# Performance work log

Hardware: AMD Instinct MI355X
Metric: run time of the kernel (lower is better)

Reference implementation:

```python
import jax, jax.numpy as jnp
import numpy as np

B, C, H, Wd = 16, 256, 64, 64
D_MODEL = 256


def setup_inputs() -> dict:
    key = jax.random.key(0)
    kx, kw = jax.random.split(key)
    x = jax.random.normal(kx, (B, C, H, Wd), dtype=jnp.float32)
    # 1x1 conv weight [out_c=1+2*d_model, in_c], scaled like kaiming-ish init
    W = jax.random.normal(kw, (1 + 2 * D_MODEL, C), dtype=jnp.float32) / np.sqrt(C)
    return {"x": x, "W": W}


def reference(x, W):
    b, c, h, w = x.shape
    d = (W.shape[0] - 1) // 2
    n = h * w
    xf = x.reshape(b, c, n)                      # [b, c, N]
    qkv = jnp.einsum('oc,bcn->bon', W, xf)       # 1x1 conv == channel GEMM
    q = qkv[:, :1]                               # [b, 1, N]
    k = qkv[:, 1:1 + d]                          # [b, d, N]
    v = qkv[:, 1 + d:]                           # [b, d, N]
    scores = jax.nn.softmax(q, axis=-1)          # softmax over tokens
    ctx = jnp.sum(k * scores, axis=-1, keepdims=True)  # [b, d, 1]
    out = jax.nn.relu(v) * ctx                   # gated ReLU(v)
    return out.reshape(b, d, h, w)
```

## Files before the change

### kernel.cpp

```cpp
#include <hip/hip_runtime.h>
#include <cstdint>
#include <cstddef>

#define NB 16
#define NC 256
#define NN 4096
#define ND 256

typedef unsigned short u16;
typedef unsigned int u32;

typedef __attribute__((ext_vector_type(8))) short short8;
typedef __attribute__((ext_vector_type(4))) float f32x4;

__device__ __forceinline__ u16 f2bf(float f) {
  union { float f; u32 u; } v; v.f = f;
  u32 r = v.u + 0x7FFFu + ((v.u >> 16) & 1u);
  return (u16)(r >> 16);
}

__global__ __launch_bounds__(256) void k_cast_transpose(const float* __restrict__ x,
                                                        u16* __restrict__ xbT) {
  __shared__ __align__(16) u16 tile[64 * 68];
  const int t = threadIdx.x;
  const int b = blockIdx.z, c0 = blockIdx.y * 64, n0 = blockIdx.x * 64;
  const float* xb = x + (size_t)(b * NC + c0) * NN + n0;
#pragma unroll
  for (int i = 0; i < 4; ++i) {
    int e = t + i * 256;
    int cl = e >> 4;
    int nl = (e & 15) * 4;
    float4 v = *(const float4*)(xb + (size_t)cl * NN + nl);
    tile[(nl + 0) * 68 + cl] = f2bf(v.x);
    tile[(nl + 1) * 68 + cl] = f2bf(v.y);
    tile[(nl + 2) * 68 + cl] = f2bf(v.z);
    tile[(nl + 3) * 68 + cl] = f2bf(v.w);
  }
  __syncthreads();
  u16* ob = xbT + (size_t)(b * NN + n0) * NC + c0;
#pragma unroll
  for (int i = 0; i < 4; ++i) {
    int e = t + i * 256;
    int nl = e >> 4;
    int cl = (e & 15) * 4;
    ushort4 pv = *(const ushort4*)&tile[nl * 68 + cl];
    *(ushort4*)(ob + (size_t)nl * NC + cl) = pv;
  }
}

__global__ __launch_bounds__(256) void k_q(const float* __restrict__ x,
                                           const float* __restrict__ W,
                                           float* __restrict__ q) {
  const int b = blockIdx.y;
  const int n = blockIdx.x * 256 + threadIdx.x;
  const float* xp = x + (size_t)b * NC * NN + n;
  float acc = 0.f;
#pragma unroll 16
  for (int c = 0; c < NC; ++c) acc += W[c] * xp[(size_t)c * NN];
  q[b * NN + n] = acc;
}

__global__ __launch_bounds__(256) void k_softmax(const float* __restrict__ q,
                                                 float* __restrict__ s) {
  __shared__ float red[256];
  const int b = blockIdx.x, t = threadIdx.x;
  const float* qb = q + b * NN;
  float v[16];
  float m = -3.4e38f;
#pragma unroll
  for (int i = 0; i < 16; ++i) { v[i] = qb[t + i * 256]; m = fmaxf(m, v[i]); }
  red[t] = m;
  __syncthreads();
  for (int off = 128; off > 0; off >>= 1) {
    if (t < off) red[t] = fmaxf(red[t], red[t + off]);
    __syncthreads();
  }
  const float M = red[0];
  __syncthreads();
  float sum = 0.f;
#pragma unroll
  for (int i = 0; i < 16; ++i) { v[i] = __expf(v[i] - M); sum += v[i]; }
  red[t] = sum;
  __syncthreads();
  for (int off = 128; off > 0; off >>= 1) {
    if (t < off) red[t] += red[t + off];
    __syncthreads();
  }
  const float inv = 1.f / red[0];
  float* sb = s + b * NN;
#pragma unroll
  for (int i = 0; i < 16; ++i) sb[t + i * 256] = v[i] * inv;
}

__global__ __launch_bounds__(256) void k_xs(const float* __restrict__ x,
                                            const float* __restrict__ s,
                                            float* __restrict__ xs) {
  __shared__ float red[256];
  const int c = blockIdx.x, b = blockIdx.y, t = threadIdx.x;
  const float* xp = x + (size_t)(b * NC + c) * NN;
  const float* sp = s + b * NN;
  float acc = 0.f;
#pragma unroll
  for (int i = 0; i < 16; ++i) { int n = t + i * 256; acc += xp[n] * sp[n]; }
  red[t] = acc;
  __syncthreads();
  for (int off = 128; off > 0; off >>= 1) {
    if (t < off) red[t] += red[t + off];
    __syncthreads();
  }
  if (t == 0) xs[b * NC + c] = red[0];
}

__global__ __launch_bounds__(256) void k_ctx(const float* __restrict__ W,
                                             const float* __restrict__ xs,
                                             float* __restrict__ ctx) {
  __shared__ float sx[NC];
  const int b = blockIdx.x, d = threadIdx.x;
  sx[d] = xs[b * NC + d];
  __syncthreads();
  const float* wk = W + (size_t)(1 + d) * NC;
  float acc = 0.f;
#pragma unroll 4
  for (int c = 0; c < NC; ++c) acc += wk[c] * sx[c];
  ctx[b * NC + d] = acc;
}

__global__ __launch_bounds__(256) void k_castwv(const float* __restrict__ W,
                                                u16* __restrict__ wvb) {
  const int i = (blockIdx.x * 256 + threadIdx.x) * 4;
  const float4 v = *(const float4*)(W + (size_t)(1 + ND) * NC + i);
  ushort4 o;
  o.x = f2bf(v.x); o.y = f2bf(v.y); o.z = f2bf(v.z); o.w = f2bf(v.w);
  *(ushort4*)(wvb + i) = o;
}

#define BM 128
#define BN 128
#define BK 32

__global__ __launch_bounds__(256) void k_gemm(const u16* __restrict__ xbT,
                                              const u16* __restrict__ wvb,
                                              const float* __restrict__ ctx,
                                              float* __restrict__ out) {
  __shared__ __align__(16) u16 As[BM * BK];
  __shared__ __align__(16) u16 Bs[BN * BK];
  const int t = threadIdx.x;
  const int b = blockIdx.z;
  const int d0 = blockIdx.y * BM;
  const int n0 = blockIdx.x * BN;
  const int lane = t & 63, w = t >> 6;
  const int wd = (w & 1) * 64, wn = (w >> 1) * 64;
  const int quad = lane >> 4, l15 = lane & 15;

  f32x4 acc[4][4];
#pragma unroll
  for (int mi = 0; mi < 4; ++mi)
#pragma unroll
    for (int ni = 0; ni < 4; ++ni)
      acc[mi][ni] = (f32x4){0.f, 0.f, 0.f, 0.f};

  const int row0 = t >> 2;
  const int qc8 = (t & 3) * 8;

  const u16* gA = wvb + (size_t)(d0 + row0) * NC + qc8;
  const u16* gB = xbT + (size_t)(b * NN + n0 + row0) * NC + qc8;
  u16* lA = &As[row0 * BK + qc8];
  u16* lB = &Bs[row0 * BK + qc8];

  for (int kk = 0; kk < NC; kk += BK) {
    __syncthreads();
#pragma unroll
    for (int i = 0; i < 2; ++i) {
      __builtin_amdgcn_global_load_lds(
          (const __attribute__((address_space(1))) u32*)(gA + kk + (size_t)(64 * i) * NC),
          (__attribute__((address_space(3))) u32*)(lA + 64 * i * BK), 16, 0, 0);
      __builtin_amdgcn_global_load_lds(
          (const __attribute__((address_space(1))) u32*)(gB + kk + (size_t)(64 * i) * NC),
          (__attribute__((address_space(3))) u32*)(lB + 64 * i * BK), 16, 0, 0);
    }
    __syncthreads();

    short8 af[4], bfr[4];
#pragma unroll
    for (int mi = 0; mi < 4; ++mi)
      af[mi] = *(const short8*)&As[(wd + mi * 16 + l15) * BK + quad * 8];
#pragma unroll
    for (int ni = 0; ni < 4; ++ni)
      bfr[ni] = *(const short8*)&Bs[(wn + ni * 16 + l15) * BK + quad * 8];
#pragma unroll
    for (int mi = 0; mi < 4; ++mi)
#pragma unroll
      for (int ni = 0; ni < 4; ++ni)
        acc[mi][ni] = __builtin_amdgcn_mfma_f32_16x16x32_bf16(af[mi], bfr[ni],
                                                              acc[mi][ni], 0, 0, 0);
  }

#pragma unroll
  for (int mi = 0; mi < 4; ++mi) {
#pragma unroll
    for (int r = 0; r < 4; ++r) {
      const int d = d0 + wd + mi * 16 + quad * 4 + r;
      const float cx = ctx[b * NC + d];
      float* op = out + (size_t)(b * NC + d) * NN + n0 + wn + l15;
#pragma unroll
      for (int ni = 0; ni < 4; ++ni) {
        float v = acc[mi][ni][r];
        op[ni * 16] = fmaxf(v, 0.f) * cx;
      }
    }
  }
}

extern "C" void kernel_launch(void* const* d_in, const int* in_sizes, int n_in,
                              void* d_out, int out_size, void* d_ws, size_t ws_size,
                              hipStream_t stream) {
  const float* x = (const float*)d_in[0];
  const float* W = (const float*)d_in[1];
  float* out = (float*)d_out;

  char* ws = (char*)d_ws;
  u16* xbT   = (u16*)ws;
  float* q   = (float*)(ws + 33554432);
  float* s   = (float*)(ws + 33554432 + 262144);
  float* xs  = (float*)(ws + 33554432 + 524288);
  float* ctx = (float*)(ws + 33554432 + 540672);
  u16* wvb   = (u16*)(ws + 33554432 + 557056);

  k_cast_transpose<<<dim3(64, 4, 16), 256, 0, stream>>>(x, xbT);
  k_q<<<dim3(16, 16), 256, 0, stream>>>(x, W, q);
  k_softmax<<<16, 256, 0, stream>>>(q, s);
  k_xs<<<dim3(256, 16), 256, 0, stream>>>(x, s, xs);
  k_ctx<<<16, 256, 0, stream>>>(W, xs, ctx);
  k_castwv<<<64, 256, 0, stream>>>(W, wvb);
  k_gemm<<<dim3(32, 2, 16), 256, 0, stream>>>(xbT, wvb, ctx, out);
}
```

Measured before the change: 175.7 us.

## Fuse q projection into cast-transpose, read bf16 xbT for xs, widen GEMM BK with swizzle

The q projection is computed inside the cast/transpose kernel from the already-loaded x tile and accumulated with atomics, so the separate pass over fp32 x is removed. The xs reduction now reads the half-size bf16 transposed copy instead of fp32 x and combines partial sums with atomics. The GEMM K-tile grows from 32 to 64 with an XOR-swizzled LDS layout, which halves the sync count and is meant to avoid bank conflicts. In exchange it adds a zeroing kernel and atomic accumulation, and xs now comes from bf16-rounded inputs, which loses some precision.

```diff
diff --git a/kernel.cpp b/kernel.cpp
--- a/kernel.cpp
+++ b/kernel.cpp
@@ -18,46 +18,58 @@
   u32 r = v.u + 0x7FFFu + ((v.u >> 16) & 1u);
   return (u16)(r >> 16);
 }
-
-__global__ __launch_bounds__(256) void k_cast_transpose(const float* __restrict__ x,
-                                                        u16* __restrict__ xbT) {
+__device__ __forceinline__ float bf2f(u16 h) {
+  union { u32 u; float f; } v; v.u = ((u32)h) << 16; return v.f;
+}
+
+__global__ __launch_bounds__(256) void k_zero(float* __restrict__ q,
+                                              float* __restrict__ xs) {
+  const int i = blockIdx.x * 256 + threadIdx.x;
+  if (i < NB * NN) q[i] = 0.f;
+  else xs[i - NB * NN] = 0.f;
+}
+
+__global__ __launch_bounds__(256) void k_cast_transpose_q(const float* __restrict__ x,
+                                                          const float* __restrict__ W,
+                                                          u16* __restrict__ xbT,
+                                                          float* __restrict__ q) {
   __shared__ __align__(16) u16 tile[64 * 68];
+  __shared__ float qred[16 * 64];
   const int t = threadIdx.x;
   const int b = blockIdx.z, c0 = blockIdx.y * 64, n0 = blockIdx.x * 64;
   const float* xb = x + (size_t)(b * NC + c0) * NN + n0;
+  const int nl = (t & 15) * 4;
+  float qacc[4] = {0.f, 0.f, 0.f, 0.f};
 #pragma unroll
   for (int i = 0; i < 4; ++i) {
-    int e = t + i * 256;
-    int cl = e >> 4;
-    int nl = (e & 15) * 4;
+    int cl = (t >> 4) + i * 16;
     float4 v = *(const float4*)(xb + (size_t)cl * NN + nl);
+    const float wq = W[c0 + cl];
+    qacc[0] += wq * v.x; qacc[1] += wq * v.y;
+    qacc[2] += wq * v.z; qacc[3] += wq * v.w;
     tile[(nl + 0) * 68 + cl] = f2bf(v.x);
     tile[(nl + 1) * 68 + cl] = f2bf(v.y);
     tile[(nl + 2) * 68 + cl] = f2bf(v.z);
     tile[(nl + 3) * 68 + cl] = f2bf(v.w);
   }
+#pragma unroll
+  for (int j = 0; j < 4; ++j) qred[(t >> 4) * 64 + nl + j] = qacc[j];
   __syncthreads();
   u16* ob = xbT + (size_t)(b * NN + n0) * NC + c0;
 #pragma unroll
   for (int i = 0; i < 4; ++i) {
     int e = t + i * 256;
-    int nl = e >> 4;
-    int cl = (e & 15) * 4;
-    ushort4 pv = *(const ushort4*)&tile[nl * 68 + cl];
-    *(ushort4*)(ob + (size_t)nl * NC + cl) = pv;
-  }
-}
-
-__global__ __launch_bounds__(256) void k_q(const float* __restrict__ x,
-                                           const float* __restrict__ W,
-                                           float* __restrict__ q) {
-  const int b = blockIdx.y;
-  const int n = blockIdx.x * 256 + threadIdx.x;
-  const float* xp = x + (size_t)b * NC * NN + n;
-  float acc = 0.f;
-#pragma unroll 16
-  for (int c = 0; c < NC; ++c) acc += W[c] * xp[(size_t)c * NN];
-  q[b * NN + n] = acc;
+    int rn = e >> 4;
+    int rc = (e & 15) * 4;
+    ushort4 pv = *(const ushort4*)&tile[rn * 68 + rc];
+    *(ushort4*)(ob + (size_t)rn * NC + rc) = pv;
+  }
+  if (t < 64) {
+    float s = 0.f;
+#pragma unroll
+    for (int k = 0; k < 16; ++k) s += qred[k * 64 + t];
+    atomicAdd(&q[b * NN + n0 + t], s);
+  }
 }
 
 __global__ __launch_bounds__(256) void k_softmax(const float* __restrict__ q,
@@ -92,23 +104,19 @@
   for (int i = 0; i < 16; ++i) sb[t + i * 256] = v[i] * inv;
 }
 
-__global__ __launch_bounds__(256) void k_xs(const float* __restrict__ x,
+__global__ __launch_bounds__(256) void k_xs(const u16* __restrict__ xbT,
                                             const float* __restrict__ s,
                                             float* __restrict__ xs) {
-  __shared__ float red[256];
-  const int c = blockIdx.x, b = blockIdx.y, t = threadIdx.x;
-  const float* xp = x + (size_t)(b * NC + c) * NN;
-  const float* sp = s + b * NN;
+  const int t = threadIdx.x;
+  const int b = blockIdx.y, n0 = blockIdx.x * 128;
+  const u16* xp = xbT + ((size_t)(b * NN + n0)) * NC + t;
+  const float* sp = s + b * NN + n0;
   float acc = 0.f;
-#pragma unroll
-  for (int i = 0; i < 16; ++i) { int n = t + i * 256; acc += xp[n] * sp[n]; }
-  red[t] = acc;
-  __syncthreads();
-  for (int off = 128; off > 0; off >>= 1) {
-    if (t < off) red[t] += red[t + off];
-    __syncthreads();
-  }
-  if (t == 0) xs[b * NC + c] = red[0];
+#pragma unroll 8
+  for (int j = 0; j < 128; ++j) {
+    acc += bf2f(xp[(size_t)j * NC]) * sp[j];
+  }
+  atomicAdd(&xs[b * NC + t], acc);
 }
 
 __global__ __launch_bounds__(256) void k_ctx(const float* __restrict__ W,
@@ -136,7 +144,7 @@
 
 #define BM 128
 #define BN 128
-#define BK 32
+#define BK 64
 
 __global__ __launch_bounds__(256) void k_gemm(const u16* __restrict__ xbT,
                                               const u16* __restrict__ wvb,
@@ -159,40 +167,45 @@
     for (int ni = 0; ni < 4; ++ni)
       acc[mi][ni] = (f32x4){0.f, 0.f, 0.f, 0.f};
 
-  const int row0 = t >> 2;
-  const int qc8 = (t & 3) * 8;
-
-  const u16* gA = wvb + (size_t)(d0 + row0) * NC + qc8;
-  const u16* gB = xbT + (size_t)(b * NN + n0 + row0) * NC + qc8;
-  u16* lA = &As[row0 * BK + qc8];
-  u16* lB = &Bs[row0 * BK + qc8];
+  const int rstg = t >> 3;
+  const int l8 = (((t & 7) ^ (rstg & 7))) * 8;
+  const u16* gA = wvb + (size_t)(d0 + rstg) * NC + l8;
+  const u16* gB = xbT + (size_t)(b * NN + n0 + rstg) * NC + l8;
+  const int ldst = 8 * t;
+
+  const int pq0 = ((0 * 4 + quad) ^ (l15 & 7)) * 8;
+  const int pq1 = ((1 * 4 + quad) ^ (l15 & 7)) * 8;
 
   for (int kk = 0; kk < NC; kk += BK) {
     __syncthreads();
 #pragma unroll
-    for (int i = 0; i < 2; ++i) {
+    for (int i = 0; i < 4; ++i) {
       __builtin_amdgcn_global_load_lds(
-          (const __attribute__((address_space(1))) u32*)(gA + kk + (size_t)(64 * i) * NC),
-          (__attribute__((address_space(3))) u32*)(lA + 64 * i * BK), 16, 0, 0);
+          (const __attribute__((address_space(1))) u32*)(gA + kk + (size_t)(32 * i) * NC),
+          (__attribute__((address_space(3))) u32*)(As + 2048 * i + ldst), 16, 0, 0);
       __builtin_amdgcn_global_load_lds(
-          (const __attribute__((address_space(1))) u32*)(gB + kk + (size_t)(64 * i) * NC),
-          (__attribute__((address_space(3))) u32*)(lB + 64 * i * BK), 16, 0, 0);
+          (const __attribute__((address_space(1))) u32*)(gB + kk + (size_t)(32 * i) * NC),
+          (__attribute__((address_space(3))) u32*)(Bs + 2048 * i + ldst), 16, 0, 0);
     }
     __syncthreads();
 
-    short8 af[4], bfr[4];
-#pragma unroll
-    for (int mi = 0; mi < 4; ++mi)
-      af[mi] = *(const short8*)&As[(wd + mi * 16 + l15) * BK + quad * 8];
-#pragma unroll
-    for (int ni = 0; ni < 4; ++ni)
-      bfr[ni] = *(const short8*)&Bs[(wn + ni * 16 + l15) * BK + quad * 8];
-#pragma unroll
-    for (int mi = 0; mi < 4; ++mi)
+#pragma unroll
+    for (int kq = 0; kq < 2; ++kq) {
+      const int pq = kq ? pq1 : pq0;
+      short8 af[4], bfr[4];
+#pragma unroll
+      for (int mi = 0; mi < 4; ++mi)
+        af[mi] = *(const short8*)&As[(wd + mi * 16 + l15) * BK + pq];
 #pragma unroll
       for (int ni = 0; ni < 4; ++ni)
-        acc[mi][ni] = __builtin_amdgcn_mfma_f32_16x16x32_bf16(af[mi], bfr[ni],
-                                                              acc[mi][ni], 0, 0, 0);
+        bfr[ni] = *(const short8*)&Bs[(wn + ni * 16 + l15) * BK + pq];
+#pragma unroll
+      for (int mi = 0; mi < 4; ++mi)
+#pragma unroll
+        for (int ni = 0; ni < 4; ++ni)
+          acc[mi][ni] = __builtin_amdgcn_mfma_f32_16x16x32_bf16(af[mi], bfr[ni],
+                                                                acc[mi][ni], 0, 0, 0);
+    }
   }
 
 #pragma unroll
@@ -226,10 +239,10 @@
   float* ctx = (float*)(ws + 33554432 + 540672);
   u16* wvb   = (u16*)(ws + 33554432 + 557056);
 
-  k_cast_transpose<<<dim3(64, 4, 16), 256, 0, stream>>>(x, xbT);
-  k_q<<<dim3(16, 16), 256, 0, stream>>>(x, W, q);
+  k_zero<<<272, 256, 0, stream>>>(q, xs);
+  k_cast_transpose_q<<<dim3(64, 4, 16), 256, 0, stream>>>(x, W, xbT, q);
   k_softmax<<<16, 256, 0, stream>>>(q, s);
-  k_xs<<<dim3(256, 16), 256, 0, stream>>>(x, s, xs);
+  k_xs<<<dim3(32, 16), 256, 0, stream>>>(xbT, s, xs);
   k_ctx<<<16, 256, 0, stream>>>(W, xs, ctx);
   k_castwv<<<64, 256, 0, stream>>>(W, wvb);
   k_gemm<<<dim3(32, 2, 16), 256, 0, stream>>>(xbT, wvb, ctx, out);
```

Result: faster. 154.2 us (-12.3%).
